# Performance work log

Hardware: AMD Instinct MI355X
Metric: run time of the kernel (lower is better)

Reference implementation:

```python
import jax, jax.numpy as jnp
import numpy as np

B, IN, H = 16384, 512, 1024

def setup_inputs() -> dict:
    key = jax.random.key(0)
    ks = jax.random.split(key, 9)
    s_h = 1.0 / np.sqrt(H)
    s_x = 1.0 / np.sqrt(IN)
    return {
        "x": jax.random.normal(ks[0], (B, IN), jnp.float32),
        "h_prev": jax.random.normal(ks[1], (B, H), jnp.float32),
        # SLIM1 gates: Linear(H->H, bias=True)
        "W_u": jax.random.uniform(ks[2], (H, H), jnp.float32, -s_h, s_h),
        "b_u": jax.random.uniform(ks[3], (H,), jnp.float32, -s_h, s_h),
        "W_r": jax.random.uniform(ks[4], (H, H), jnp.float32, -s_h, s_h),
        "b_r": jax.random.uniform(ks[5], (H,), jnp.float32, -s_h, s_h),
        # hidden candidate: Linear(IN->H, bias=False) and Linear(H->H, bias=True)
        "W_hx": jax.random.uniform(ks[6], (H, IN), jnp.float32, -s_x, s_x),
        "W_hh": jax.random.uniform(ks[7], (H, H), jnp.float32, -s_h, s_h),
        "b_h": jax.random.uniform(ks[8], (H,), jnp.float32, -s_h, s_h),
    }

def reference(x, h_prev, W_u, b_u, W_r, b_r, W_hx, W_hh, b_h):
    # update and reset gates depend only on h_prev (SLIM1: sigmoid(W h + b))
    u = jax.nn.sigmoid(h_prev @ W_u.T + b_u)          # [B, H]
    r = jax.nn.sigmoid(h_prev @ W_r.T + b_r)          # [B, H]
    # candidate hidden state: tanh(W_hx x + W_hh (r*h) + b)
    h_cand = jnp.tanh(x @ W_hx.T + (r * h_prev) @ W_hh.T + b_h)  # [B, H]
    h_next = (1.0 - u) * h_prev + u * h_cand
    return (h_next, h_next)
```

## Files before the change

### kernel.cpp

```cpp
#include <hip/hip_runtime.h>
#include <hip/hip_bf16.h>

#define M_DIM 16384
#define IN_DIM 512
#define H_DIM 1024
#define BH (M_DIM * H_DIM)
#define K2 1536

typedef float f32x4 __attribute__((ext_vector_type(4)));
typedef short bf16x8 __attribute__((ext_vector_type(8)));

static __device__ __forceinline__ unsigned short f2bf(float f) {
    union { float f; unsigned u; } a; a.f = f;
    unsigned r = a.u + 0x7fffu + ((a.u >> 16) & 1u);
    return (unsigned short)(r >> 16);
}
static __device__ __forceinline__ float bf2f(unsigned short u) {
    union { unsigned u; float f; } a; a.u = (unsigned)u << 16;
    return a.f;
}

#define OFF_HB   0u
#define OFF_A2   16777216u
#define OFF_WU   41943040u
#define OFF_WR   42991616u
#define OFF_W2   44040192u
#define OFF_U16  45613056u
#define WS2_ELEMS 62390272u
#define WS2_NEED_BYTES (WS2_ELEMS * 2ull)

__global__ __launch_bounds__(256) void k_conv(const float* __restrict__ x,
                                              const float* __restrict__ h,
                                              const float* __restrict__ wu,
                                              const float* __restrict__ whx,
                                              const float* __restrict__ whh,
                                              const float* __restrict__ wr,
                                              unsigned short* __restrict__ ws) {
    const int total = 3604480;
    for (int u = blockIdx.x * blockDim.x + threadIdx.x; u < total;
         u += gridDim.x * blockDim.x) {
        const float* src; unsigned short* d; int lu;
        if (u < 2097152)      { lu = u;
                                src = h + (size_t)lu * 8;
                                d = ws + OFF_HB + (size_t)lu * 8; }
        else if (u < 3145728) { lu = u - 2097152;
                                src = x + (size_t)lu * 8;
                                d = ws + OFF_A2 + (size_t)(lu >> 6) * K2 + (lu & 63) * 8; }
        else if (u < 3276800) { lu = u - 3145728;
                                src = wu + (size_t)lu * 8;
                                d = ws + OFF_WU + (size_t)lu * 8; }
        else if (u < 3342336) { lu = u - 3276800;
                                src = whx + (size_t)lu * 8;
                                d = ws + OFF_W2 + (size_t)(lu >> 6) * K2 + (lu & 63) * 8; }
        else if (u < 3473408) { lu = u - 3342336;
                                src = whh + (size_t)lu * 8;
                                d = ws + OFF_W2 + (size_t)(lu >> 7) * K2 + 512 + (lu & 127) * 8; }
        else                  { lu = u - 3473408;
                                src = wr + (size_t)lu * 8;
                                d = ws + OFF_WR + (size_t)lu * 8; }
        float4 a = *reinterpret_cast<const float4*>(src);
        float4 b = *reinterpret_cast<const float4*>(src + 4);
        uint4 p;
        p.x = (unsigned)f2bf(a.x) | ((unsigned)f2bf(a.y) << 16);
        p.y = (unsigned)f2bf(a.z) | ((unsigned)f2bf(a.w) << 16);
        p.z = (unsigned)f2bf(b.x) | ((unsigned)f2bf(b.y) << 16);
        p.w = (unsigned)f2bf(b.z) | ((unsigned)f2bf(b.w) << 16);
        *reinterpret_cast<uint4*>(d) = p;
    }
}

static __device__ __forceinline__ void stage_lds(const unsigned short* __restrict__ src,
                                                 int rowBase, int ld, int ks,
                                                 unsigned short* lds, int tid) {
#pragma unroll
    for (int i = 0; i < 4; ++i) {
        int c = i * 256 + tid;
        int r = c >> 3, kc = c & 7;
        int gc = kc ^ (r & 7);
        const unsigned short* g = src + (size_t)(rowBase + r) * ld + ks + gc * 8;
        unsigned short* l = lds + c * 8;
        __builtin_amdgcn_global_load_lds((const __attribute__((address_space(1))) void*)g,
                                         (__attribute__((address_space(3))) void*)l,
                                         16, 0, 0);
    }
}

template <int KSEG>
static __device__ __forceinline__ void gemm_seg(const unsigned short* __restrict__ A, int aLd,
                                                const unsigned short* __restrict__ B, int bLd,
                                                int bm, int bn,
                                                unsigned short* As, unsigned short* Bs,
                                                int tid, int wm, int wn, int frow, int klane,
                                                f32x4 acc[4][4]) {
    for (int ks = 0; ks < KSEG; ks += 64) {
        stage_lds(A, bm * 128, aLd, ks, As, tid);
        stage_lds(B, bn * 128, bLd, ks, Bs, tid);
        __syncthreads();
#pragma unroll
        for (int kk = 0; kk < 2; ++kk) {
            bf16x8 av[4], bv[4];
#pragma unroll
            for (int m = 0; m < 4; ++m) {
                int pr = wm * 64 + m * 16 + frow;
                av[m] = *reinterpret_cast<const bf16x8*>(
                    &As[pr * 64 + (((kk << 2) + klane) ^ (pr & 7)) * 8]);
            }
#pragma unroll
            for (int n = 0; n < 4; ++n) {
                int pr = wn * 64 + n * 16 + frow;
                bv[n] = *reinterpret_cast<const bf16x8*>(
                    &Bs[pr * 64 + (((kk << 2) + klane) ^ (pr & 7)) * 8]);
            }
#pragma unroll
            for (int m = 0; m < 4; ++m)
#pragma unroll
                for (int n = 0; n < 4; ++n)
                    acc[m][n] = __builtin_amdgcn_mfma_f32_16x16x32_bf16(av[m], bv[n], acc[m][n], 0, 0, 0);
        }
        __syncthreads();
    }
}

__global__ __launch_bounds__(256, 4) void k_rgate_s(const unsigned short* __restrict__ hb,
                                                    const unsigned short* __restrict__ wrb,
                                                    const float* __restrict__ b_r,
                                                    unsigned short* __restrict__ rhA2) {
    __shared__ unsigned short As[128 * 64];
    __shared__ unsigned short Bs[128 * 64];

    int bid = blockIdx.x;
    int swz = (bid & 7) * 128 + (bid >> 3);
    int bm = swz >> 3, bn = swz & 7;

    int tid = threadIdx.x;
    int wave = tid >> 6, lane = tid & 63;
    int wm = wave >> 1, wn = wave & 1;
    int frow = lane & 15, klane = lane >> 4;

    f32x4 acc[4][4] = {};
    gemm_seg<H_DIM>(hb, H_DIM, wrb, H_DIM, bm, bn, As, Bs, tid, wm, wn, frow, klane, acc);

    int rbase = bm * 128 + wm * 64;
    int cbase = bn * 128 + wn * 64;
#pragma unroll
    for (int m = 0; m < 4; ++m) {
#pragma unroll
        for (int n = 0; n < 4; ++n) {
            int col = cbase + n * 16 + frow;
            float bs = b_r[col];
#pragma unroll
            for (int q = 0; q < 4; ++q) {
                int row = rbase + m * 16 + klane * 4 + q;
                float g = 1.0f / (1.0f + __expf(-(acc[m][n][q] + bs)));
                rhA2[(size_t)row * K2 + col] = f2bf(g * bf2f(hb[(size_t)row * H_DIM + col]));
            }
        }
    }
}

__global__ __launch_bounds__(256, 4) void k_ugate_s(const unsigned short* __restrict__ hb,
                                                    const unsigned short* __restrict__ wub,
                                                    const float* __restrict__ b_u,
                                                    unsigned short* __restrict__ u16) {
    __shared__ unsigned short As[128 * 64];
    __shared__ unsigned short Bs[128 * 64];

    int bid = blockIdx.x;
    int swz = (bid & 7) * 128 + (bid >> 3);
    int bm = swz >> 3, bn = swz & 7;

    int tid = threadIdx.x;
    int wave = tid >> 6, lane = tid & 63;
    int wm = wave >> 1, wn = wave & 1;
    int frow = lane & 15, klane = lane >> 4;

    f32x4 acc[4][4] = {};
    gemm_seg<H_DIM>(hb, H_DIM, wub, H_DIM, bm, bn, As, Bs, tid, wm, wn, frow, klane, acc);

    int rbase = bm * 128 + wm * 64;
    int cbase = bn * 128 + wn * 64;
#pragma unroll
    for (int m = 0; m < 4; ++m) {
#pragma unroll
        for (int n = 0; n < 4; ++n) {
            int col = cbase + n * 16 + frow;
            float bs = b_u[col];
#pragma unroll
            for (int q = 0; q < 4; ++q) {
                int row = rbase + m * 16 + klane * 4 + q;
                float g = 1.0f / (1.0f + __expf(-(acc[m][n][q] + bs)));
                u16[(size_t)row * H_DIM + col] = f2bf(g);
            }
        }
    }
}

__global__ __launch_bounds__(256, 4) void k_cand_b(const unsigned short* __restrict__ a2,
                                                   const unsigned short* __restrict__ w2,
                                                   const unsigned short* __restrict__ hb,
                                                   const unsigned short* __restrict__ u16,
                                                   const float* __restrict__ b_h,
                                                   float* __restrict__ out) {
    __shared__ unsigned short As[128 * 64];
    __shared__ unsigned short Bs[128 * 64];

    int bid = blockIdx.x;
    int swz = (bid & 7) * 128 + (bid >> 3);
    int bm = swz >> 3, bn = swz & 7;

    int tid = threadIdx.x;
    int wave = tid >> 6, lane = tid & 63;
    int wm = wave >> 1, wn = wave & 1;
    int frow = lane & 15, klane = lane >> 4;

    f32x4 acc[4][4] = {};
    gemm_seg<K2>(a2, K2, w2, K2, bm, bn, As, Bs, tid, wm, wn, frow, klane, acc);

    int rbase = bm * 128 + wm * 64;
    int cbase = bn * 128 + wn * 64;
#pragma unroll
    for (int m = 0; m < 4; ++m) {
#pragma unroll
        for (int n = 0; n < 4; ++n) {
            int col = cbase + n * 16 + frow;
            float bh = b_h[col];
#pragma unroll
            for (int q = 0; q < 4; ++q) {
                int row = rbase + m * 16 + klane * 4 + q;
                size_t off = (size_t)row * H_DIM + col;
                float hp = bf2f(hb[off]);
                float u = bf2f(u16[off]);
                float cpre = acc[m][n][q] + bh;
                cpre = fminf(fmaxf(cpre, -15.0f), 15.0f);
                float e = __expf(2.0f * cpre);
                float c = (e - 1.0f) / (e + 1.0f);
                float h = hp + u * (c - hp);
                out[off] = h;
                out[BH + off] = h;
            }
        }
    }
}

#define LDSS 40

static __device__ __forceinline__ void stage_f32(const float* __restrict__ src, int rowBase,
                                                 int ld, int kBase,
                                                 unsigned short* lds, int tid) {
#pragma unroll
    for (int i = 0; i < 4; ++i) {
        int idx = i * 256 + tid;
        int r = idx >> 3, c4 = idx & 7;
        const float4 v = *reinterpret_cast<const float4*>(
            src + (size_t)(rowBase + r) * ld + kBase + c4 * 4);
        uint2 p;
        p.x = (unsigned)f2bf(v.x) | ((unsigned)f2bf(v.y) << 16);
        p.y = (unsigned)f2bf(v.z) | ((unsigned)f2bf(v.w) << 16);
        *reinterpret_cast<uint2*>(lds + r * LDSS + c4 * 4) = p;
    }
}

static __device__ __forceinline__ void stage_bf16s(const unsigned short* __restrict__ src,
                                                   int rowBase, int ld, int kBase,
                                                   unsigned short* lds, int tid) {
#pragma unroll
    for (int i = 0; i < 2; ++i) {
        int idx = i * 256 + tid;
        int r = idx >> 2, c8 = idx & 3;
        const uint4 v = *reinterpret_cast<const uint4*>(
            src + (size_t)(rowBase + r) * ld + kBase + c8 * 8);
        *reinterpret_cast<uint4*>(lds + r * LDSS + c8 * 8) = v;
    }
}

__global__ __launch_bounds__(256, 2) void k_rgate(const float* __restrict__ h_prev,
                                                  const float* __restrict__ W_r,
                                                  const float* __restrict__ b_r,
                                                  unsigned short* __restrict__ rh) {
    __shared__ unsigned short As[128 * LDSS];
    __shared__ unsigned short Bs[128 * LDSS];
    int bid = blockIdx.x;
    int swz = (bid & 7) * 128 + (bid >> 3);
    int bm = swz >> 3, bn = swz & 7;
    int tid = threadIdx.x;
    int wave = tid >> 6, lane = tid & 63;
    int wm = wave >> 1, wn = wave & 1;
    int frow = lane & 15, koff = (lane >> 4) * 8;
    f32x4 acc[4][4] = {};
    for (int ks = 0; ks < H_DIM; ks += 32) {
        stage_f32(h_prev, bm * 128, H_DIM, ks, As, tid);
        stage_f32(W_r, bn * 128, H_DIM, ks, Bs, tid);
        __syncthreads();
        bf16x8 av[4], bv[4];
#pragma unroll
        for (int m = 0; m < 4; ++m)
            av[m] = *reinterpret_cast<const bf16x8*>(&As[(wm * 64 + m * 16 + frow) * LDSS + koff]);
#pragma unroll
        for (int n = 0; n < 4; ++n)
            bv[n] = *reinterpret_cast<const bf16x8*>(&Bs[(wn * 64 + n * 16 + frow) * LDSS + koff]);
#pragma unroll
        for (int m = 0; m < 4; ++m)
#pragma unroll
            for (int n = 0; n < 4; ++n)
                acc[m][n] = __builtin_amdgcn_mfma_f32_16x16x32_bf16(av[m], bv[n], acc[m][n], 0, 0, 0);
        __syncthreads();
    }
    int rbase = bm * 128 + wm * 64, cbase = bn * 128 + wn * 64;
#pragma unroll
    for (int m = 0; m < 4; ++m)
#pragma unroll
        for (int n = 0; n < 4; ++n) {
            int col = cbase + n * 16 + frow;
            float bias = b_r[col];
#pragma unroll
            for (int q = 0; q < 4; ++q) {
                int row = rbase + m * 16 + (lane >> 4) * 4 + q;
                float pre = acc[m][n][q] + bias;
                float rv = 1.0f / (1.0f + __expf(-pre));
                rh[(size_t)row * H_DIM + col] = f2bf(rv * h_prev[(size_t)row * H_DIM + col]);
            }
        }
}

__global__ __launch_bounds__(256, 2) void k_fused(const float* __restrict__ x,
                                                  const float* __restrict__ h_prev,
                                                  const float* __restrict__ W_u,
                                                  const float* __restrict__ b_u,
                                                  const float* __restrict__ W_hx,
                                                  const float* __restrict__ W_hh,
                                                  const float* __restrict__ b_h,
                                                  const unsigned short* __restrict__ rh,
                                                  float* __restrict__ out) {
    __shared__ unsigned short As[128 * LDSS];
    __shared__ unsigned short Bs[128 * LDSS];
    int bid = blockIdx.x;
    int swz = (bid & 7) * 128 + (bid >> 3);
    int bm = swz >> 3, bn = swz & 7;
    int tid = threadIdx.x;
    int wave = tid >> 6, lane = tid & 63;
    int wm = wave >> 1, wn = wave & 1;
    int frow = lane & 15, koff = (lane >> 4) * 8;
    f32x4 accu[4][4] = {};
    f32x4 accc[4][4] = {};
    for (int ks = 0; ks < H_DIM; ks += 32) {
        stage_f32(h_prev, bm * 128, H_DIM, ks, As, tid);
        stage_f32(W_u, bn * 128, H_DIM, ks, Bs, tid);
        __syncthreads();
        bf16x8 av[4], bv[4];
#pragma unroll
        for (int m = 0; m < 4; ++m)
            av[m] = *reinterpret_cast<const bf16x8*>(&As[(wm * 64 + m * 16 + frow) * LDSS + koff]);
#pragma unroll
        for (int n = 0; n < 4; ++n)
            bv[n] = *reinterpret_cast<const bf16x8*>(&Bs[(wn * 64 + n * 16 + frow) * LDSS + koff]);
#pragma unroll
        for (int m = 0; m < 4; ++m)
#pragma unroll
            for (int n = 0; n < 4; ++n)
                accu[m][n] = __builtin_amdgcn_mfma_f32_16x16x32_bf16(av[m], bv[n], accu[m][n], 0, 0, 0);
        __syncthreads();
    }
    for (int ks = 0; ks < IN_DIM; ks += 32) {
        stage_f32(x, bm * 128, IN_DIM, ks, As, tid);
        stage_f32(W_hx, bn * 128, IN_DIM, ks, Bs, tid);
        __syncthreads();
        bf16x8 av[4], bv[4];
#pragma unroll
        for (int m = 0; m < 4; ++m)
            av[m] = *reinterpret_cast<const bf16x8*>(&As[(wm * 64 + m * 16 + frow) * LDSS + koff]);
#pragma unroll
        for (int n = 0; n < 4; ++n)
            bv[n] = *reinterpret_cast<const bf16x8*>(&Bs[(wn * 64 + n * 16 + frow) * LDSS + koff]);
#pragma unroll
        for (int m = 0; m < 4; ++m)
#pragma unroll
            for (int n = 0; n < 4; ++n)
                accc[m][n] = __builtin_amdgcn_mfma_f32_16x16x32_bf16(av[m], bv[n], accc[m][n], 0, 0, 0);
        __syncthreads();
    }
    for (int ks = 0; ks < H_DIM; ks += 32) {
        stage_bf16s(rh, bm * 128, H_DIM, ks, As, tid);
        stage_f32(W_hh, bn * 128, H_DIM, ks, Bs, tid);
        __syncthreads();
        bf16x8 av[4], bv[4];
#pragma unroll
        for (int m = 0; m < 4; ++m)
            av[m] = *reinterpret_cast<const bf16x8*>(&As[(wm * 64 + m * 16 + frow) * LDSS + koff]);
#pragma unroll
        for (int n = 0; n < 4; ++n)
            bv[n] = *reinterpret_cast<const bf16x8*>(&Bs[(wn * 64 + n * 16 + frow) * LDSS + koff]);
#pragma unroll
        for (int m = 0; m < 4; ++m)
#pragma unroll
            for (int n = 0; n < 4; ++n)
                accc[m][n] = __builtin_amdgcn_mfma_f32_16x16x32_bf16(av[m], bv[n], accc[m][n], 0, 0, 0);
        __syncthreads();
    }
    int rbase = bm * 128 + wm * 64, cbase = bn * 128 + wn * 64;
#pragma unroll
    for (int m = 0; m < 4; ++m)
#pragma unroll
        for (int n = 0; n < 4; ++n) {
            int col = cbase + n * 16 + frow;
            float bu = b_u[col], bh = b_h[col];
#pragma unroll
            for (int q = 0; q < 4; ++q) {
                int row = rbase + m * 16 + (lane >> 4) * 4 + q;
                size_t off = (size_t)row * H_DIM + col;
                float hp = h_prev[off];
                float u = 1.0f / (1.0f + __expf(-(accu[m][n][q] + bu)));
                float cpre = accc[m][n][q] + bh;
                cpre = fminf(fmaxf(cpre, -15.0f), 15.0f);
                float e = __expf(2.0f * cpre);
                float c = (e - 1.0f) / (e + 1.0f);
                float h = hp + u * (c - hp);
                out[off] = h;
                out[BH + off] = h;
            }
        }
}

extern "C" void kernel_launch(void* const* d_in, const int* in_sizes, int n_in,
                              void* d_out, int out_size, void* d_ws, size_t ws_size,
                              hipStream_t stream) {
    const float* x      = (const float*)d_in[0];
    const float* h_prev = (const float*)d_in[1];
    const float* W_u    = (const float*)d_in[2];
    const float* b_u    = (const float*)d_in[3];
    const float* W_r    = (const float*)d_in[4];
    const float* b_r    = (const float*)d_in[5];
    const float* W_hx   = (const float*)d_in[6];
    const float* W_hh   = (const float*)d_in[7];
    const float* b_h    = (const float*)d_in[8];
    float* out = (float*)d_out;

    if (ws_size >= WS2_NEED_BYTES) {
        unsigned short* ws = (unsigned short*)d_ws;
        hipLaunchKernelGGL(k_conv, dim3(2048), dim3(256), 0, stream,
                           x, h_prev, W_u, W_hx, W_hh, W_r, ws);
        hipLaunchKernelGGL(k_rgate_s, dim3(1024), dim3(256), 0, stream,
                           ws + OFF_HB, ws + OFF_WR, b_r, ws + OFF_A2 + 512);
        hipLaunchKernelGGL(k_ugate_s, dim3(1024), dim3(256), 0, stream,
                           ws + OFF_HB, ws + OFF_WU, b_u, ws + OFF_U16);
        hipLaunchKernelGGL(k_cand_b, dim3(1024), dim3(256), 0, stream,
                           ws + OFF_A2, ws + OFF_W2, ws + OFF_HB, ws + OFF_U16,
                           b_h, out);
    } else {
        unsigned short* rh = (unsigned short*)d_ws;
        hipLaunchKernelGGL(k_rgate, dim3(1024), dim3(256), 0, stream, h_prev, W_r, b_r, rh);
        hipLaunchKernelGGL(k_fused, dim3(1024), dim3(256), 0, stream,
                           x, h_prev, W_u, b_u, W_hx, W_hh, b_h, rh, out);
    }
}
```

Baseline: 187.0 us.

## Rewrite candidate GEMM as 256x256-tile, 8-wave kernel with direct-to-LDS double buffering

The candidate-state GEMM kernel moves from a 128x128 tile with 4 waves to a 256x256 tile with 8 waves per block. Operands are loaded straight into a swizzled, double-buffered LDS region with global_load_lds, and quarter-tile loads are interleaved with MFMA phases under raised wave priority. The aim is higher operand reuse per loaded byte and overlap of global loads with matrix math. In exchange it uses 128 KB of LDS and one block per CU, and only 256 blocks are launched, so CU utilisation and tail balance depend on the grid fitting the device.

```diff
diff --git a/kernel.cpp b/kernel.cpp
--- a/kernel.cpp
+++ b/kernel.cpp
@@ -195,42 +195,152 @@
     }
 }
 
-__global__ __launch_bounds__(256, 4) void k_cand_b(const unsigned short* __restrict__ a2,
+template <int NT>
+static __device__ __forceinline__ void gemm8(const unsigned short* __restrict__ A, int aLd,
+                                             const unsigned short* __restrict__ B, int bLd,
+                                             int bm, int bn, unsigned short* L, int tid,
+                                             int wm, int wn, int frow, int klane,
+                                             f32x4 acc[8][4]) {
+    auto stage = [&](const unsigned short* src, int rowBase, int ld, int kt,
+                     unsigned short* region) {
+#pragma unroll
+        for (int i = 0; i < 2; ++i) {
+            int c = i * 512 + tid;
+            int rp = c >> 3, kc = c & 7;
+            int gc = kc ^ (rp & 7);
+            const unsigned short* g = src + (size_t)(rowBase + rp) * ld + kt * 64 + gc * 8;
+            __builtin_amdgcn_global_load_lds((const __attribute__((address_space(1))) void*)g,
+                                             (__attribute__((address_space(3))) void*)(region + c * 8),
+                                             16, 0, 0);
+        }
+    };
+
+    const int bhalf = wn >> 1;
+    const int brow0 = (wn & 1) * 64;
+
+    bf16x8 av[4][2], bv[2][2];
+
+    auto rdA = [&](unsigned short* Lb, int mh) {
+#pragma unroll
+        for (int mf = 0; mf < 4; ++mf)
+#pragma unroll
+            for (int kk = 0; kk < 2; ++kk) {
+                int r = mh * 64 + mf * 16 + frow;
+                av[mf][kk] = *reinterpret_cast<const bf16x8*>(
+                    &Lb[wm * 8192 + r * 64 + (((kk << 2) + klane) ^ (r & 7)) * 8]);
+            }
+    };
+    auto rdB = [&](unsigned short* Lb, int nh) {
+#pragma unroll
+        for (int nf = 0; nf < 2; ++nf)
+#pragma unroll
+            for (int kk = 0; kk < 2; ++kk) {
+                int r = brow0 + nh * 32 + nf * 16 + frow;
+                bv[nf][kk] = *reinterpret_cast<const bf16x8*>(
+                    &Lb[16384 + bhalf * 8192 + r * 64 + (((kk << 2) + klane) ^ (r & 7)) * 8]);
+            }
+    };
+    auto mf16 = [&](int mh, int nh) {
+        __builtin_amdgcn_s_setprio(1);
+#pragma unroll
+        for (int kk = 0; kk < 2; ++kk)
+#pragma unroll
+            for (int mf = 0; mf < 4; ++mf)
+#pragma unroll
+                for (int nf = 0; nf < 2; ++nf)
+                    acc[mh * 4 + mf][nh * 2 + nf] = __builtin_amdgcn_mfma_f32_16x16x32_bf16(
+                        av[mf][kk], bv[nf][kk], acc[mh * 4 + mf][nh * 2 + nf], 0, 0, 0);
+        __builtin_amdgcn_s_setprio(0);
+    };
+
+    stage(A, bm * 256,       aLd, 0, L);
+    stage(A, bm * 256 + 128, aLd, 0, L + 8192);
+    stage(B, bn * 256,       bLd, 0, L + 16384);
+    stage(B, bn * 256 + 128, bLd, 0, L + 24576);
+    asm volatile("s_waitcnt vmcnt(0)" ::: "memory");
+    __builtin_amdgcn_s_barrier();
+
+    for (int g = 0; g < NT - 1; ++g) {
+        unsigned short* Lb = L + (g & 1) * 32768;
+        unsigned short* Ln = L + ((g & 1) ^ 1) * 32768;
+        rdA(Lb, 0); rdB(Lb, 0);
+        stage(A, bm * 256, aLd, g + 1, Ln);
+        __builtin_amdgcn_s_barrier();
+        mf16(0, 0);
+        __builtin_amdgcn_s_barrier();
+        rdB(Lb, 1);
+        stage(B, bn * 256, bLd, g + 1, Ln + 16384);
+        __builtin_amdgcn_s_barrier();
+        mf16(0, 1);
+        asm volatile("s_waitcnt vmcnt(4)" ::: "memory");
+        __builtin_amdgcn_s_barrier();
+        rdA(Lb, 1); rdB(Lb, 0);
+        stage(A, bm * 256 + 128, aLd, g + 1, Ln + 8192);
+        __builtin_amdgcn_s_barrier();
+        mf16(1, 0);
+        __builtin_amdgcn_s_barrier();
+        rdB(Lb, 1);
+        stage(B, bn * 256 + 128, bLd, g + 1, Ln + 24576);
+        __builtin_amdgcn_s_barrier();
+        mf16(1, 1);
+        asm volatile("s_waitcnt vmcnt(4)" ::: "memory");
+        __builtin_amdgcn_s_barrier();
+    }
+    {
+        unsigned short* Lb = L + ((NT - 1) & 1) * 32768;
+        rdA(Lb, 0); rdB(Lb, 0);
+        __builtin_amdgcn_s_barrier();
+        mf16(0, 0);
+        __builtin_amdgcn_s_barrier();
+        rdB(Lb, 1);
+        __builtin_amdgcn_s_barrier();
+        mf16(0, 1);
+        asm volatile("s_waitcnt vmcnt(0)" ::: "memory");
+        __builtin_amdgcn_s_barrier();
+        rdA(Lb, 1); rdB(Lb, 0);
+        __builtin_amdgcn_s_barrier();
+        mf16(1, 0);
+        __builtin_amdgcn_s_barrier();
+        rdB(Lb, 1);
+        __builtin_amdgcn_s_barrier();
+        mf16(1, 1);
+    }
+}
+
+__global__ __launch_bounds__(512, 1) void k_cand_8(const unsigned short* __restrict__ a2,
                                                    const unsigned short* __restrict__ w2,
                                                    const unsigned short* __restrict__ hb,
                                                    const unsigned short* __restrict__ u16,
                                                    const float* __restrict__ b_h,
                                                    float* __restrict__ out) {
-    __shared__ unsigned short As[128 * 64];
-    __shared__ unsigned short Bs[128 * 64];
-
+    __shared__ unsigned short L[65536];
     int bid = blockIdx.x;
-    int swz = (bid & 7) * 128 + (bid >> 3);
-    int bm = swz >> 3, bn = swz & 7;
+    int swz = (bid & 7) * 32 + (bid >> 3);
+    int bm = swz >> 2, bn = swz & 3;
 
     int tid = threadIdx.x;
     int wave = tid >> 6, lane = tid & 63;
-    int wm = wave >> 1, wn = wave & 1;
+    int wm = wave >> 2, wn = wave & 3;
     int frow = lane & 15, klane = lane >> 4;
 
-    f32x4 acc[4][4] = {};
-    gemm_seg<K2>(a2, K2, w2, K2, bm, bn, As, Bs, tid, wm, wn, frow, klane, acc);
-
-    int rbase = bm * 128 + wm * 64;
-    int cbase = bn * 128 + wn * 64;
-#pragma unroll
-    for (int m = 0; m < 4; ++m) {
+    f32x4 acc[8][4] = {};
+    gemm8<24>(a2, K2, w2, K2, bm, bn, L, tid, wm, wn, frow, klane, acc);
+
+    int rbase = bm * 256 + wm * 128;
+    int cbase = bn * 256 + wn * 64;
+#pragma unroll
+    for (int a = 0; a < 8; ++a) {
 #pragma unroll
         for (int n = 0; n < 4; ++n) {
-            int col = cbase + n * 16 + frow;
+            int col = cbase + (n >> 1) * 32 + (n & 1) * 16 + frow;
             float bh = b_h[col];
 #pragma unroll
             for (int q = 0; q < 4; ++q) {
-                int row = rbase + m * 16 + klane * 4 + q;
+                int row = rbase + (a >> 2) * 64 + (a & 3) * 16 + klane * 4 + q;
                 size_t off = (size_t)row * H_DIM + col;
                 float hp = bf2f(hb[off]);
                 float u = bf2f(u16[off]);
-                float cpre = acc[m][n][q] + bh;
+                float cpre = acc[a][n][q] + bh;
                 cpre = fminf(fmaxf(cpre, -15.0f), 15.0f);
                 float e = __expf(2.0f * cpre);
                 float c = (e - 1.0f) / (e + 1.0f);
@@ -442,7 +552,7 @@
                            ws + OFF_HB, ws + OFF_WR, b_r, ws + OFF_A2 + 512);
         hipLaunchKernelGGL(k_ugate_s, dim3(1024), dim3(256), 0, stream,
                            ws + OFF_HB, ws + OFF_WU, b_u, ws + OFF_U16);
-        hipLaunchKernelGGL(k_cand_b, dim3(1024), dim3(256), 0, stream,
+        hipLaunchKernelGGL(k_cand_8, dim3(256), dim3(512), 0, stream,
                            ws + OFF_A2, ws + OFF_W2, ws + OFF_HB, ws + OFF_U16,
                            b_h, out);
     } else {
```

Result: slower. 195.0 us (+4.3%).
